# Kernel tuning notes

Measured on AMD Instinct MI355X. Metric: run time of the kernel, lower is better.

## Reference

```python
import jax, jax.numpy as jnp
import numpy as np
from jax import lax

B, T_ENC, IN, H, V, EMB = 128, 512, 2, 256, 29, 8


def _gru_cell(x_t, h, Wih, Whh, bih, bhh):
    # PyTorch GRU cell, gate order (r, z, n)
    gi = x_t @ Wih.T + bih            # [B, 3H]
    gh = h @ Whh.T + bhh              # [B, 3H]
    ir, iz, inn = jnp.split(gi, 3, axis=-1)
    hr, hz, hn = jnp.split(gh, 3, axis=-1)
    r = jax.nn.sigmoid(ir + hr)
    z = jax.nn.sigmoid(iz + hz)
    n = jnp.tanh(inn + r * hn)
    return (1.0 - z) * n + z * h


def _gru_scan(xs, Wih, Whh, bih, bhh, reverse):
    # xs: [B, T, D] -> outputs [B, T, H], final hidden [B, H]
    h0 = jnp.zeros((xs.shape[0], Whh.shape[-1]), xs.dtype)
    def step(h, x_t):
        h = _gru_cell(x_t, h, Wih, Whh, bih, bhh)
        return h, h
    hT, ys = lax.scan(step, h0, jnp.swapaxes(xs, 0, 1), reverse=reverse)
    return jnp.swapaxes(ys, 0, 1), hT


def _forward(x, target_seq, eWih0, eWhh0, ebih0, ebhh0, eWih1, eWhh1, ebih1, ebhh1,
             e2d_W, e2d_b, dWih0, dWih1, dWhh, dbih, dbhh, q_W, q_b, out_W, out_b, emb):
    # ---- bidirectional 2-layer GRU encoder ----
    yf0, hf0 = _gru_scan(x, eWih0[0], eWhh0[0], ebih0[0], ebhh0[0], False)
    yb0, hb0 = _gru_scan(x, eWih0[1], eWhh0[1], ebih0[1], ebhh0[1], True)
    y0 = jnp.concatenate([yf0, yb0], axis=-1)          # [B, T, 2H]
    yf1, hf1 = _gru_scan(y0, eWih1[0], eWhh1[0], ebih1[0], ebhh1[0], False)
    yb1, hb1 = _gru_scan(y0, eWih1[1], eWhh1[1], ebih1[1], ebhh1[1], True)
    y1 = jnp.concatenate([yf1, yb1], axis=-1)          # [B, T, 2H]
    enc_out = y1 @ e2d_W.T + e2d_b                     # [B, T, H]
    # hidden.reshape(L, 2, B, H).sum(dim=1): fwd + bwd per layer
    h0c = hf0 + hb0
    h1c = hf1 + hb1

    max_steps = target_seq.shape[1] - 1
    init_tok = target_seq[:, 0]

    def dec_step(carry, _):
        h0, h1, tok = carry
        e = emb[tok]                                   # [B, EMB]
        h0 = _gru_cell(e, h0, dWih0, dWhh[0], dbih[0], dbhh[0])
        h1 = _gru_cell(h0, h1, dWih1, dWhh[1], dbih[1], dbhh[1])
        q = h1 @ q_W.T + q_b                           # [B, H]
        scores = jnp.einsum('bte,be->bt', enc_out, q)  # [B, T]
        w = jax.nn.softmax(scores, axis=1)
        ctx = jnp.einsum('bt,bte->be', w, enc_out)     # [B, H]
        logits = (h1 + ctx) @ out_W.T + out_b          # [B, V] (dropout is identity in eval)
        tok = jnp.argmax(logits, axis=-1)
        return (h0, h1, tok), logits

    (h0c, h1c, _), logits = lax.scan(dec_step, (h0c, h1c, init_tok), None, length=max_steps)
    logits = jnp.swapaxes(logits, 0, 1)                # [B, max_steps, V]
    hidden = jnp.stack([h0c, h1c], axis=0)             # [L, B, H]
    return logits, hidden


def setup_inputs() -> dict:
    key = jax.random.key(0)
    ks = jax.random.split(key, 24)
    def p(k, *shape):
        return jax.random.normal(k, shape, jnp.float32) * 0.05
    return {
        'x': jax.random.normal(ks[0], (B, T_ENC, IN), jnp.float32),
        'target_seq': jax.random.randint(ks[1], (B, 64), 0, V),
        'eWih0': p(ks[2], 2, 3 * H, IN),
        'eWhh0': p(ks[3], 2, 3 * H, H),
        'ebih0': p(ks[4], 2, 3 * H),
        'ebhh0': p(ks[5], 2, 3 * H),
        'eWih1': p(ks[6], 2, 3 * H, 2 * H),
        'eWhh1': p(ks[7], 2, 3 * H, H),
        'ebih1': p(ks[8], 2, 3 * H),
        'ebhh1': p(ks[9], 2, 3 * H),
        'e2d_W': p(ks[10], H, 2 * H),
        'e2d_b': p(ks[11], H),
        'dWih0': p(ks[12], 3 * H, EMB),
        'dWih1': p(ks[13], 3 * H, H),
        'dWhh': p(ks[14], 2, 3 * H, H),
        'dbih': p(ks[15], 2, 3 * H),
        'dbhh': p(ks[16], 2, 3 * H),
        'q_W': p(ks[17], H, H),
        'q_b': p(ks[18], H),
        'out_W': p(ks[19], V, H),
        'out_b': p(ks[20], V),
        'emb': p(ks[21], V, EMB),
    }


def reference(x, target_seq, eWih0, eWhh0, ebih0, ebhh0, eWih1, eWhh1, ebih1, ebhh1,
              e2d_W, e2d_b, dWih0, dWih1, dWhh, dbih, dbhh, q_W, q_b, out_W, out_b, emb):
    return _forward(x, target_seq, eWih0, eWhh0, ebih0, ebhh0, eWih1, eWhh1, ebih1, ebhh1,
                    e2d_W, e2d_b, dWih0, dWih1, dWhh, dbih, dbhh, q_W, q_b, out_W, out_b, emb)
```

## Files before the change

kernel.cpp:

```cpp
#include <hip/hip_runtime.h>
#include <hip/hip_bf16.h>
#include <hip/hip_fp16.h>
#include <stdint.h>

#define BB 128
#define TT 512
#define HH 256
#define VV 29
#define NSTEP 63
#define BT (BB*TT)
#define CHUNK 64

typedef _Float16 f16;
typedef _Float16 f16x2 __attribute__((ext_vector_type(2)));
typedef _Float16 f16x8 __attribute__((ext_vector_type(8)));
typedef float f32x4 __attribute__((ext_vector_type(4)));

static __device__ __forceinline__ float fdot2u(uint32_t a, uint32_t b, float c) {
  return __builtin_amdgcn_fdot2(__builtin_bit_cast(f16x2, a),
                                __builtin_bit_cast(f16x2, b), c, false);
}
static __device__ __forceinline__ float sigm_(float x) {
  return 1.0f / (1.0f + __expf(-x));
}

__global__ void k_cvt(const float* __restrict__ s, f16* __restrict__ d, int n) {
  int i = blockIdx.x * 256 + threadIdx.x;
  if (i < n) d[i] = (f16)s[i];
}

template<int LAYER>
__global__ __launch_bounds__(512, 2)
void k_scan(const float* __restrict__ x,
            const f16* __restrict__ gi,
            const uint32_t* __restrict__ whh,
            const float* __restrict__ wih0,
            const float* __restrict__ bih,
            const float* __restrict__ bhh,
            f16* __restrict__ y,
            float* __restrict__ hstate,
            int t0, int nsteps)
{
  const int wg = blockIdx.x, b = wg >> 1, dir = wg & 1;
  const int tid = threadIdx.x, pair = tid >> 1, half = tid & 1;
  __shared__ uint32_t hv[128];
  __shared__ float ysh[256];

  uint32_t w0[64], w1[64], w2[64];
  {
    const uint32_t* wp = whh + (size_t)dir * 768 * 128;
    const uint32_t* r0 = wp + (size_t)pair * 128 + half * 64;
    const uint32_t* r1 = wp + (size_t)(pair + 256) * 128 + half * 64;
    const uint32_t* r2 = wp + (size_t)(pair + 512) * 128 + half * 64;
#pragma unroll
    for (int i = 0; i < 64; i++) { w0[i] = r0[i]; w1[i] = r1[i]; w2[i] = r2[i]; }
  }
  const float bh0 = bhh[dir * 768 + pair];
  const float bh1 = bhh[dir * 768 + pair + 256];
  const float bh2 = bhh[dir * 768 + pair + 512];
  float bi0 = 0, bi1 = 0, bi2 = 0;
  float wi00 = 0, wi01 = 0, wi10 = 0, wi11 = 0, wi20 = 0, wi21 = 0;
  if (LAYER == 0) {
    bi0 = bih[dir * 768 + pair];
    bi1 = bih[dir * 768 + pair + 256];
    bi2 = bih[dir * 768 + pair + 512];
    wi00 = wih0[(dir * 768 + pair) * 2 + 0];
    wi01 = wih0[(dir * 768 + pair) * 2 + 1];
    wi10 = wih0[(dir * 768 + pair + 256) * 2 + 0];
    wi11 = wih0[(dir * 768 + pair + 256) * 2 + 1];
    wi20 = wih0[(dir * 768 + pair + 512) * 2 + 0];
    wi21 = wih0[(dir * 768 + pair + 512) * 2 + 1];
  }
  float* hs = hstate + ((size_t)dir * BB + b) * 256;
  float hreg = hs[pair];
  if (tid < 128) {
    f16x2 p2; p2[0] = (f16)hs[2 * tid]; p2[1] = (f16)hs[2 * tid + 1];
    hv[tid] = __builtin_bit_cast(uint32_t, p2);
  }
  __syncthreads();

  for (int s = 0; s < nsteps; ++s) {
    const int t = dir ? (TT - 1 - t0 - s) : (t0 + s);
    float a0 = 0.f, a1 = 0.f, a2 = 0.f;
#pragma unroll
    for (int i = 0; i < 64; i++) {
      uint32_t hh = hv[half * 64 + i];
      a0 = fdot2u(w0[i], hh, a0);
      a1 = fdot2u(w1[i], hh, a1);
      a2 = fdot2u(w2[i], hh, a2);
    }
    a0 += __shfl_xor(a0, 1);
    a1 += __shfl_xor(a1, 1);
    a2 += __shfl_xor(a2, 1);

    float gr, gz, gn;
    if (LAYER == 0) {
      float x0 = x[((size_t)b * TT + t) * 2 + 0];
      float x1 = x[((size_t)b * TT + t) * 2 + 1];
      gr = wi00 * x0 + wi01 * x1 + bi0;
      gz = wi10 * x0 + wi11 * x1 + bi1;
      gn = wi20 * x0 + wi21 * x1 + bi2;
    } else {
      const f16* g = gi + ((size_t)b * nsteps + s) * 1536 + dir * 768 + pair;
      gr = (float)g[0]; gz = (float)g[256]; gn = (float)g[512];
    }
    float r = sigm_(gr + a0 + bh0);
    float z = sigm_(gz + a1 + bh1);
    float n = tanhf(gn + r * (a2 + bh2));
    float hn = (1.0f - z) * n + z * hreg;
    hreg = hn;
    __syncthreads();
    if (half == 0) { ((f16*)hv)[pair] = (f16)hn; ysh[pair] = hn; }
    __syncthreads();
    if (tid < 256) y[((size_t)b * TT + t) * 512 + dir * 256 + tid] = (f16)ysh[tid];
  }
  if (half == 0) hs[pair] = hreg;
}

__global__ __launch_bounds__(256)
void k_gemm(const f16* __restrict__ A, const f16* __restrict__ Bt,
            f16* __restrict__ C, const float* __restrict__ bias,
            int K, int shift, long bstride, int inner, int ldc, int coloff)
{
  const int m0 = blockIdx.x * 64, n0 = blockIdx.y * 64;
  const int tid = threadIdx.x, lane = tid & 63, wv = tid >> 6;
  __shared__ __align__(16) f16 As[64 * 40];
  __shared__ __align__(16) f16 Bs[64 * 40];
  f32x4 acc[4] = {{0,0,0,0},{0,0,0,0},{0,0,0,0},{0,0,0,0}};
  const int lrow = tid >> 2, lseg = tid & 3;
  const int ml = lane & 15, quad = lane >> 4;
  const int r = m0 + lrow;
  const f16* arow = A + (long)(r >> shift) * bstride
                      + (long)(r & ((1 << shift) - 1)) * inner;
  const f16* brow = Bt + (size_t)(n0 + lrow) * K;
  for (int k0 = 0; k0 < K; k0 += 32) {
    uint4 av = *(const uint4*)(arow + k0 + lseg * 8);
    uint4 bv = *(const uint4*)(brow + k0 + lseg * 8);
    __syncthreads();
    *(uint4*)(As + lrow * 40 + lseg * 8) = av;
    *(uint4*)(Bs + lrow * 40 + lseg * 8) = bv;
    __syncthreads();
    f16x8 af = *(const f16x8*)(As + (wv * 16 + ml) * 40 + quad * 8);
#pragma unroll
    for (int ns = 0; ns < 4; ++ns) {
      f16x8 bf = *(const f16x8*)(Bs + (ns * 16 + ml) * 40 + quad * 8);
      acc[ns] = __builtin_amdgcn_mfma_f32_16x16x32_f16(af, bf, acc[ns], 0, 0, 0);
    }
  }
#pragma unroll
  for (int ns = 0; ns < 4; ++ns) {
#pragma unroll
    for (int rr = 0; rr < 4; ++rr) {
      int row = m0 + wv * 16 + quad * 4 + rr;
      int col = n0 + ns * 16 + ml;
      float v = acc[ns][rr];
      if (bias) v += bias[col];
      C[(size_t)row * ldc + coloff + col] = (f16)v;
    }
  }
}

__global__ void k_dinit(const float* __restrict__ hf0, const float* __restrict__ hf1,
                        const int* __restrict__ tseq,
                        f16* __restrict__ h0, f16* __restrict__ h1, int* __restrict__ tok) {
  int i = blockIdx.x * 256 + threadIdx.x;
  h0[i] = (f16)(hf0[i] + hf0[32768 + i]);
  h1[i] = (f16)(hf1[i] + hf1[32768 + i]);
  if (i < BB) tok[i] = tseq[i * 64];
}

__global__ __launch_bounds__(256)
void k_gates0(const f16* __restrict__ wih0,
              const float* __restrict__ bih0,
              const float* __restrict__ emb,
              const int* __restrict__ tok,
              const f16* __restrict__ G,
              const f16* __restrict__ hprev, f16* __restrict__ hnew) {
  int b = blockIdx.x, p = threadIdx.x;
  __shared__ float e[8];
  if (p < 8) e[p] = emb[tok[b] * 8 + p];
  __syncthreads();
  float gr = bih0[p], gz = bih0[p + 256], gn = bih0[p + 512];
#pragma unroll
  for (int i = 0; i < 8; i++) {
    gr += e[i] * (float)wih0[p * 8 + i];
    gz += e[i] * (float)wih0[(p + 256) * 8 + i];
    gn += e[i] * (float)wih0[(p + 512) * 8 + i];
  }
  const f16* g = G + b * 768;
  float r = sigm_(gr + (float)g[p]);
  float z = sigm_(gz + (float)g[p + 256]);
  float n = tanhf(gn + r * (float)g[p + 512]);
  float hp = (float)hprev[b * 256 + p];
  hnew[b * 256 + p] = (f16)((1.f - z) * n + z * hp);
}

__global__ __launch_bounds__(256)
void k_gates1(const f16* __restrict__ Ga, const f16* __restrict__ Gb,
              const f16* __restrict__ hprev, f16* __restrict__ hnew) {
  int b = blockIdx.x, p = threadIdx.x;
  const f16* ga = Ga + b * 768;
  const f16* gb = Gb + b * 768;
  float r = sigm_((float)ga[p] + (float)gb[p]);
  float z = sigm_((float)ga[p + 256] + (float)gb[p + 256]);
  float n = tanhf((float)ga[p + 512] + r * (float)gb[p + 512]);
  float hp = (float)hprev[b * 256 + p];
  hnew[b * 256 + p] = (f16)((1.f - z) * n + z * hp);
}

__global__ __launch_bounds__(256)
void k_attn(const f16* __restrict__ enc,
            const f16* __restrict__ q,
            const f16* __restrict__ h1,
            const f16* __restrict__ outw,
            const float* __restrict__ outb,
            float* __restrict__ dlogits, int* __restrict__ tok, int step) {
  int b = blockIdx.x, tid = threadIdx.x;
  __shared__ uint32_t qs[128];
  __shared__ float sc[512];
  __shared__ float red[4];
  __shared__ float hc[256];
  __shared__ float lg[32];
  if (tid < 128) qs[tid] = ((const uint32_t*)q)[b * 128 + tid];
  __syncthreads();
#pragma unroll
  for (int pass = 0; pass < 2; ++pass) {
    int t = tid + pass * 256;
    const uint4* ep = (const uint4*)(enc + ((size_t)b * TT + t) * 256);
    float s = 0.f;
#pragma unroll
    for (int j = 0; j < 32; j++) {
      uint4 v = ep[j];
      s = fdot2u(v.x, qs[j * 4 + 0], s);
      s = fdot2u(v.y, qs[j * 4 + 1], s);
      s = fdot2u(v.z, qs[j * 4 + 2], s);
      s = fdot2u(v.w, qs[j * 4 + 3], s);
    }
    sc[t] = s;
  }
  __syncthreads();
  float mloc = fmaxf(sc[tid], sc[tid + 256]);
#pragma unroll
  for (int off = 32; off; off >>= 1) mloc = fmaxf(mloc, __shfl_xor(mloc, off));
  if ((tid & 63) == 0) red[tid >> 6] = mloc;
  __syncthreads();
  float m = fmaxf(fmaxf(red[0], red[1]), fmaxf(red[2], red[3]));
  float e0 = __expf(sc[tid] - m), e1 = __expf(sc[tid + 256] - m);
  __syncthreads();
  sc[tid] = e0; sc[tid + 256] = e1;
  float lloc = e0 + e1;
#pragma unroll
  for (int off = 32; off; off >>= 1) lloc += __shfl_xor(lloc, off);
  if ((tid & 63) == 0) red[tid >> 6] = lloc;
  __syncthreads();
  float l = red[0] + red[1] + red[2] + red[3];
  float ctx = 0.f;
#pragma unroll 4
  for (int t = 0; t < TT; t++) ctx += sc[t] * (float)enc[((size_t)b * TT + t) * 256 + tid];
  ctx /= l;
  hc[tid] = ctx + (float)h1[b * 256 + tid];
  __syncthreads();
  if (tid < VV) {
    float acc = outb[tid];
    const f16* ow = outw + tid * 256;
    for (int k = 0; k < 256; k++) acc += hc[k] * (float)ow[k];
    lg[tid] = acc;
    dlogits[((size_t)b * NSTEP + step) * VV + tid] = acc;
  }
  __syncthreads();
  if (tid == 0) {
    int best = 0; float bv = lg[0];
    for (int v = 1; v < VV; ++v) if (lg[v] > bv) { bv = lg[v]; best = v; }
    tok[b] = best;
  }
}

__global__ void k_fin(const f16* __restrict__ h0, const f16* __restrict__ h1,
                      float* __restrict__ out) {
  int i = blockIdx.x * 256 + threadIdx.x;
  out[233856 + i] = (float)(i < 32768 ? h0[i] : h1[i - 32768]);
}

extern "C" void kernel_launch(void* const* d_in, const int* in_sizes, int n_in,
                              void* d_out, int out_size, void* d_ws, size_t ws_size,
                              hipStream_t stream) {
  (void)in_sizes; (void)n_in; (void)out_size; (void)ws_size;
  const float* x     = (const float*)d_in[0];
  const int*   tseq  = (const int*)d_in[1];
  const float* eWih0 = (const float*)d_in[2];
  const float* eWhh0 = (const float*)d_in[3];
  const float* ebih0 = (const float*)d_in[4];
  const float* ebhh0 = (const float*)d_in[5];
  const float* eWih1 = (const float*)d_in[6];
  const float* eWhh1 = (const float*)d_in[7];
  const float* ebih1 = (const float*)d_in[8];
  const float* ebhh1 = (const float*)d_in[9];
  const float* e2dW  = (const float*)d_in[10];
  const float* e2db  = (const float*)d_in[11];
  const float* dWih0 = (const float*)d_in[12];
  const float* dWih1 = (const float*)d_in[13];
  const float* dWhh  = (const float*)d_in[14];
  const float* dbih  = (const float*)d_in[15];
  const float* dbhh  = (const float*)d_in[16];
  const float* qW    = (const float*)d_in[17];
  const float* qb    = (const float*)d_in[18];
  const float* outW  = (const float*)d_in[19];
  const float* outb  = (const float*)d_in[20];
  const float* emb   = (const float*)d_in[21];

  uint8_t* ws = (uint8_t*)d_ws;
  size_t o = 0;
  auto take = [&](size_t bytes) -> void* {
    void* p = ws + o;
    o += (bytes + 255) & ~(size_t)255;
    return p;
  };
  f16* whh0_16  = (f16*)take((size_t)2 * 768 * 256 * 2);
  f16* whh1_16  = (f16*)take((size_t)2 * 768 * 256 * 2);
  f16* wih1_16  = (f16*)take((size_t)2 * 768 * 512 * 2);
  f16* e2d_16   = (f16*)take((size_t)256 * 512 * 2);
  f16* qw_16    = (f16*)take((size_t)256 * 256 * 2);
  f16* outw_16  = (f16*)take((size_t)29 * 256 * 2);
  f16* dwih0_16 = (f16*)take((size_t)768 * 8 * 2);
  f16* dwih1_16 = (f16*)take((size_t)768 * 256 * 2);
  f16* dwhh_16  = (f16*)take((size_t)2 * 768 * 256 * 2);
  f16* y0   = (f16*)take((size_t)BT * 512 * 2);
  f16* y1   = (f16*)take((size_t)BT * 512 * 2);
  f16* gi   = (f16*)take((size_t)BB * CHUNK * 1536 * 2);
  float* hs0 = (float*)take((size_t)2 * BB * 256 * 4);
  float* hs1 = (float*)take((size_t)2 * BB * 256 * 4);
  f16* qbuf = (f16*)take((size_t)BB * 256 * 2);
  f16* h0buf[2] = { (f16*)take((size_t)BB * 256 * 2), (f16*)take((size_t)BB * 256 * 2) };
  f16* h1buf[2] = { (f16*)take((size_t)BB * 256 * 2), (f16*)take((size_t)BB * 256 * 2) };
  f16* G0  = (f16*)take((size_t)BB * 768 * 2);
  f16* G1a = (f16*)take((size_t)BB * 768 * 2);
  f16* G1b = (f16*)take((size_t)BB * 768 * 2);
  int* tok = (int*)take((size_t)BB * 4);
  f16* enc = y0;

  hipMemsetAsync(hs0, 0, (size_t)2 * BB * 256 * 4, stream);
  hipMemsetAsync(hs1, 0, (size_t)2 * BB * 256 * 4, stream);

  auto cvt = [&](const float* s, f16* d, int n) {
    k_cvt<<<(n + 255) / 256, 256, 0, stream>>>(s, d, n);
  };
  cvt(eWhh0, whh0_16, 2 * 768 * 256);
  cvt(eWhh1, whh1_16, 2 * 768 * 256);
  cvt(eWih1, wih1_16, 2 * 768 * 512);
  cvt(e2dW,  e2d_16,  256 * 512);
  cvt(qW,    qw_16,   256 * 256);
  cvt(outW,  outw_16, 29 * 256);
  cvt(dWih0, dwih0_16, 768 * 8);
  cvt(dWih1, dwih1_16, 768 * 256);
  cvt(dWhh,  dwhh_16, 2 * 768 * 256);

  k_scan<0><<<256, 512, 0, stream>>>(x, nullptr, (const uint32_t*)whh0_16,
                                     eWih0, ebih0, ebhh0, y0, hs0, 0, TT);

  const long BSTR = (long)TT * 512;
  for (int c = 0; c < TT / CHUNK; ++c) {
    const int t0 = c * CHUNK;
    k_gemm<<<dim3(BB * CHUNK / 64, 12), 256, 0, stream>>>(
        y0 + (size_t)t0 * 512, wih1_16, gi, ebih1,
        512, 6, BSTR, 512, 1536, 0);
    k_gemm<<<dim3(BB * CHUNK / 64, 12), 256, 0, stream>>>(
        y0 + (size_t)(TT - 1 - t0) * 512, wih1_16 + (size_t)768 * 512, gi, ebih1 + 768,
        512, 6, BSTR, -512, 1536, 768);
    k_scan<1><<<256, 512, 0, stream>>>(nullptr, gi, (const uint32_t*)whh1_16,
                                       nullptr, nullptr, ebhh1, y1, hs1, t0, CHUNK);
  }

  k_gemm<<<dim3(BT / 64, 4), 256, 0, stream>>>(y1, e2d_16, enc, e2db,
                                               512, 30, 0, 512, 256, 0);
  k_dinit<<<128, 256, 0, stream>>>(hs0, hs1, tseq, h0buf[0], h1buf[0], tok);

  int cur = 0;
  for (int s = 0; s < NSTEP; ++s) {
    int nxt = cur ^ 1;
    k_gemm<<<dim3(2, 12), 256, 0, stream>>>(h0buf[cur], dwhh_16, G0, dbhh,
                                            256, 30, 0, 256, 768, 0);
    k_gates0<<<128, 256, 0, stream>>>(dwih0_16, dbih, emb, tok, G0,
                                      h0buf[cur], h0buf[nxt]);
    k_gemm<<<dim3(2, 12), 256, 0, stream>>>(h0buf[nxt], dwih1_16, G1a, dbih + 768,
                                            256, 30, 0, 256, 768, 0);
    k_gemm<<<dim3(2, 12), 256, 0, stream>>>(h1buf[cur], dwhh_16 + (size_t)768 * 256,
                                            G1b, dbhh + 768, 256, 30, 0, 256, 768, 0);
    k_gates1<<<128, 256, 0, stream>>>(G1a, G1b, h1buf[cur], h1buf[nxt]);
    k_gemm<<<dim3(2, 4), 256, 0, stream>>>(h1buf[nxt], qw_16, qbuf, qb,
                                           256, 30, 0, 256, 256, 0);
    k_attn<<<128, 256, 0, stream>>>(enc, qbuf, h1buf[nxt], outw_16, outb,
                                    (float*)d_out, tok, s);
    cur = nxt;
  }
  k_fin<<<256, 256, 0, stream>>>(h0buf[cur], h1buf[cur], (float*)d_out);
}
```

Baseline: 6.358 ms.

## Fuse decoder loop into one persistent kernel and vectorize encoder scan

The whole 63-step autoregressive decoder (GRU cells, query projection, attention, output logits, argmax) moves into a single kernel with one block per batch row. This replaces roughly 440 small launches and the global round-trips of gates and hidden states between them. In exchange, every block re-reads the full decoder weight matrices from global/L2 each step with matrix-vector dot products instead of MFMA GEMMs. The encoder scan also switches to uint4 weight registers and vector LDS reads, and writes y directly, dropping one shared staging buffer.

```diff
diff --git a/kernel.cpp b/kernel.cpp
--- a/kernel.cpp
+++ b/kernel.cpp
@@ -43,17 +43,16 @@
 {
   const int wg = blockIdx.x, b = wg >> 1, dir = wg & 1;
   const int tid = threadIdx.x, pair = tid >> 1, half = tid & 1;
-  __shared__ uint32_t hv[128];
-  __shared__ float ysh[256];
-
-  uint32_t w0[64], w1[64], w2[64];
+  __shared__ __align__(16) uint4 hv4[32];
+
+  uint4 w0[16], w1[16], w2[16];
   {
     const uint32_t* wp = whh + (size_t)dir * 768 * 128;
-    const uint32_t* r0 = wp + (size_t)pair * 128 + half * 64;
-    const uint32_t* r1 = wp + (size_t)(pair + 256) * 128 + half * 64;
-    const uint32_t* r2 = wp + (size_t)(pair + 512) * 128 + half * 64;
-#pragma unroll
-    for (int i = 0; i < 64; i++) { w0[i] = r0[i]; w1[i] = r1[i]; w2[i] = r2[i]; }
+    const uint4* r0 = (const uint4*)(wp + (size_t)pair * 128 + half * 64);
+    const uint4* r1 = (const uint4*)(wp + (size_t)(pair + 256) * 128 + half * 64);
+    const uint4* r2 = (const uint4*)(wp + (size_t)(pair + 512) * 128 + half * 64);
+#pragma unroll
+    for (int i = 0; i < 16; i++) { w0[i] = r0[i]; w1[i] = r1[i]; w2[i] = r2[i]; }
   }
   const float bh0 = bhh[dir * 768 + pair];
   const float bh1 = bhh[dir * 768 + pair + 256];
@@ -75,24 +74,13 @@
   float hreg = hs[pair];
   if (tid < 128) {
     f16x2 p2; p2[0] = (f16)hs[2 * tid]; p2[1] = (f16)hs[2 * tid + 1];
-    hv[tid] = __builtin_bit_cast(uint32_t, p2);
+    ((uint32_t*)hv4)[tid] = __builtin_bit_cast(uint32_t, p2);
   }
   __syncthreads();
 
+  const uint4* hw = hv4 + half * 16;
   for (int s = 0; s < nsteps; ++s) {
     const int t = dir ? (TT - 1 - t0 - s) : (t0 + s);
-    float a0 = 0.f, a1 = 0.f, a2 = 0.f;
-#pragma unroll
-    for (int i = 0; i < 64; i++) {
-      uint32_t hh = hv[half * 64 + i];
-      a0 = fdot2u(w0[i], hh, a0);
-      a1 = fdot2u(w1[i], hh, a1);
-      a2 = fdot2u(w2[i], hh, a2);
-    }
-    a0 += __shfl_xor(a0, 1);
-    a1 += __shfl_xor(a1, 1);
-    a2 += __shfl_xor(a2, 1);
-
     float gr, gz, gn;
     if (LAYER == 0) {
       float x0 = x[((size_t)b * TT + t) * 2 + 0];
@@ -104,15 +92,30 @@
       const f16* g = gi + ((size_t)b * nsteps + s) * 1536 + dir * 768 + pair;
       gr = (float)g[0]; gz = (float)g[256]; gn = (float)g[512];
     }
+    float a0 = 0.f, a1 = 0.f, a2 = 0.f;
+#pragma unroll
+    for (int j = 0; j < 16; ++j) {
+      uint4 hh = hw[j];
+      a0 = fdot2u(w0[j].x, hh.x, a0); a0 = fdot2u(w0[j].y, hh.y, a0);
+      a0 = fdot2u(w0[j].z, hh.z, a0); a0 = fdot2u(w0[j].w, hh.w, a0);
+      a1 = fdot2u(w1[j].x, hh.x, a1); a1 = fdot2u(w1[j].y, hh.y, a1);
+      a1 = fdot2u(w1[j].z, hh.z, a1); a1 = fdot2u(w1[j].w, hh.w, a1);
+      a2 = fdot2u(w2[j].x, hh.x, a2); a2 = fdot2u(w2[j].y, hh.y, a2);
+      a2 = fdot2u(w2[j].z, hh.z, a2); a2 = fdot2u(w2[j].w, hh.w, a2);
+    }
+    a0 += __shfl_xor(a0, 1);
+    a1 += __shfl_xor(a1, 1);
+    a2 += __shfl_xor(a2, 1);
+
     float r = sigm_(gr + a0 + bh0);
     float z = sigm_(gz + a1 + bh1);
     float n = tanhf(gn + r * (a2 + bh2));
     float hn = (1.0f - z) * n + z * hreg;
     hreg = hn;
-    __syncthreads();
-    if (half == 0) { ((f16*)hv)[pair] = (f16)hn; ysh[pair] = hn; }
-    __syncthreads();
-    if (tid < 256) y[((size_t)b * TT + t) * 512 + dir * 256 + tid] = (f16)ysh[tid];
+    if (half == 0) y[((size_t)b * TT + t) * 512 + dir * 256 + pair] = (f16)hn;
+    __syncthreads();
+    if (half == 0) ((f16*)hv4)[pair] = (f16)hn;
+    __syncthreads();
   }
   if (half == 0) hs[pair] = hreg;
 }
@@ -160,125 +163,203 @@
   }
 }
 
-__global__ void k_dinit(const float* __restrict__ hf0, const float* __restrict__ hf1,
-                        const int* __restrict__ tseq,
-                        f16* __restrict__ h0, f16* __restrict__ h1, int* __restrict__ tok) {
-  int i = blockIdx.x * 256 + threadIdx.x;
-  h0[i] = (f16)(hf0[i] + hf0[32768 + i]);
-  h1[i] = (f16)(hf1[i] + hf1[32768 + i]);
-  if (i < BB) tok[i] = tseq[i * 64];
+static __device__ __forceinline__ void mv3(const f16* __restrict__ W, int row0,
+                                           const uint4* __restrict__ hsh,
+                                           float& g0, float& g1, float& g2) {
+  const uint4* w0 = (const uint4*)(W + (size_t)row0 * 256);
+  const uint4* w1 = (const uint4*)(W + (size_t)(row0 + 256) * 256);
+  const uint4* w2 = (const uint4*)(W + (size_t)(row0 + 512) * 256);
+#pragma unroll 2
+  for (int kc = 0; kc < 8; ++kc) {
+    uint4 hq[4], aq[4], bq[4], cq[4];
+#pragma unroll
+    for (int j = 0; j < 4; ++j) {
+      aq[j] = w0[4 * kc + j]; bq[j] = w1[4 * kc + j]; cq[j] = w2[4 * kc + j];
+      hq[j] = hsh[4 * kc + j];
+    }
+#pragma unroll
+    for (int j = 0; j < 4; ++j) {
+      g0 = fdot2u(aq[j].x, hq[j].x, g0); g0 = fdot2u(aq[j].y, hq[j].y, g0);
+      g0 = fdot2u(aq[j].z, hq[j].z, g0); g0 = fdot2u(aq[j].w, hq[j].w, g0);
+      g1 = fdot2u(bq[j].x, hq[j].x, g1); g1 = fdot2u(bq[j].y, hq[j].y, g1);
+      g1 = fdot2u(bq[j].z, hq[j].z, g1); g1 = fdot2u(bq[j].w, hq[j].w, g1);
+      g2 = fdot2u(cq[j].x, hq[j].x, g2); g2 = fdot2u(cq[j].y, hq[j].y, g2);
+      g2 = fdot2u(cq[j].z, hq[j].z, g2); g2 = fdot2u(cq[j].w, hq[j].w, g2);
+    }
+  }
+}
+static __device__ __forceinline__ float mv1(const f16* __restrict__ W, long row,
+                                            const uint4* __restrict__ hsh, float g) {
+  const uint4* w = (const uint4*)(W + (size_t)row * 256);
+#pragma unroll 2
+  for (int kc = 0; kc < 8; ++kc) {
+    uint4 aq[4], hq[4];
+#pragma unroll
+    for (int j = 0; j < 4; ++j) { aq[j] = w[4 * kc + j]; hq[j] = hsh[4 * kc + j]; }
+#pragma unroll
+    for (int j = 0; j < 4; ++j) {
+      g = fdot2u(aq[j].x, hq[j].x, g); g = fdot2u(aq[j].y, hq[j].y, g);
+      g = fdot2u(aq[j].z, hq[j].z, g); g = fdot2u(aq[j].w, hq[j].w, g);
+    }
+  }
+  return g;
+}
+static __device__ __forceinline__ float edot(uint4 w, const float* e) {
+  f16x2 a = __builtin_bit_cast(f16x2, w.x);
+  f16x2 b = __builtin_bit_cast(f16x2, w.y);
+  f16x2 c = __builtin_bit_cast(f16x2, w.z);
+  f16x2 d = __builtin_bit_cast(f16x2, w.w);
+  return (float)a[0]*e[0] + (float)a[1]*e[1] + (float)b[0]*e[2] + (float)b[1]*e[3]
+       + (float)c[0]*e[4] + (float)c[1]*e[5] + (float)d[0]*e[6] + (float)d[1]*e[7];
 }
 
 __global__ __launch_bounds__(256)
-void k_gates0(const f16* __restrict__ wih0,
-              const float* __restrict__ bih0,
-              const float* __restrict__ emb,
-              const int* __restrict__ tok,
-              const f16* __restrict__ G,
-              const f16* __restrict__ hprev, f16* __restrict__ hnew) {
-  int b = blockIdx.x, p = threadIdx.x;
-  __shared__ float e[8];
-  if (p < 8) e[p] = emb[tok[b] * 8 + p];
-  __syncthreads();
-  float gr = bih0[p], gz = bih0[p + 256], gn = bih0[p + 512];
-#pragma unroll
-  for (int i = 0; i < 8; i++) {
-    gr += e[i] * (float)wih0[p * 8 + i];
-    gz += e[i] * (float)wih0[(p + 256) * 8 + i];
-    gn += e[i] * (float)wih0[(p + 512) * 8 + i];
-  }
-  const f16* g = G + b * 768;
-  float r = sigm_(gr + (float)g[p]);
-  float z = sigm_(gz + (float)g[p + 256]);
-  float n = tanhf(gn + r * (float)g[p + 512]);
-  float hp = (float)hprev[b * 256 + p];
-  hnew[b * 256 + p] = (f16)((1.f - z) * n + z * hp);
-}
-
-__global__ __launch_bounds__(256)
-void k_gates1(const f16* __restrict__ Ga, const f16* __restrict__ Gb,
-              const f16* __restrict__ hprev, f16* __restrict__ hnew) {
-  int b = blockIdx.x, p = threadIdx.x;
-  const f16* ga = Ga + b * 768;
-  const f16* gb = Gb + b * 768;
-  float r = sigm_((float)ga[p] + (float)gb[p]);
-  float z = sigm_((float)ga[p + 256] + (float)gb[p + 256]);
-  float n = tanhf((float)ga[p + 512] + r * (float)gb[p + 512]);
-  float hp = (float)hprev[b * 256 + p];
-  hnew[b * 256 + p] = (f16)((1.f - z) * n + z * hp);
-}
-
-__global__ __launch_bounds__(256)
-void k_attn(const f16* __restrict__ enc,
-            const f16* __restrict__ q,
-            const f16* __restrict__ h1,
-            const f16* __restrict__ outw,
-            const float* __restrict__ outb,
-            float* __restrict__ dlogits, int* __restrict__ tok, int step) {
-  int b = blockIdx.x, tid = threadIdx.x;
-  __shared__ uint32_t qs[128];
+void k_decoder(const f16* __restrict__ dwhh,
+               const f16* __restrict__ dwih1,
+               const f16* __restrict__ dwih0,
+               const f16* __restrict__ qw,
+               const f16* __restrict__ outw,
+               const f16* __restrict__ enc,
+               const float* __restrict__ dbih,
+               const float* __restrict__ dbhh,
+               const float* __restrict__ qb, const float* __restrict__ outb,
+               const float* __restrict__ emb,
+               const float* __restrict__ hs0, const float* __restrict__ hs1,
+               const int* __restrict__ tseq,
+               float* __restrict__ out)
+{
+  const int b = blockIdx.x, tid = threadIdx.x;
+  __shared__ __align__(16) f16 h0sh[256], h1sh[256], qsh[256];
   __shared__ float sc[512];
   __shared__ float red[4];
-  __shared__ float hc[256];
+  __shared__ __align__(16) float hc[256];
+  __shared__ __align__(16) float cpart[2][256];
   __shared__ float lg[32];
-  if (tid < 128) qs[tid] = ((const uint32_t*)q)[b * 128 + tid];
+  __shared__ float e8[8];
+  __shared__ int toksh;
+
+  h0sh[tid] = (f16)(hs0[b * 256 + tid] + hs0[32768 + b * 256 + tid]);
+  h1sh[tid] = (f16)(hs1[b * 256 + tid] + hs1[32768 + b * 256 + tid]);
+  if (tid == 0) toksh = tseq[b * 64];
   __syncthreads();
-#pragma unroll
-  for (int pass = 0; pass < 2; ++pass) {
-    int t = tid + pass * 256;
-    const uint4* ep = (const uint4*)(enc + ((size_t)b * TT + t) * 256);
-    float s = 0.f;
-#pragma unroll
-    for (int j = 0; j < 32; j++) {
-      uint4 v = ep[j];
-      s = fdot2u(v.x, qs[j * 4 + 0], s);
-      s = fdot2u(v.y, qs[j * 4 + 1], s);
-      s = fdot2u(v.z, qs[j * 4 + 2], s);
-      s = fdot2u(v.w, qs[j * 4 + 3], s);
-    }
-    sc[t] = s;
-  }
-  __syncthreads();
-  float mloc = fmaxf(sc[tid], sc[tid + 256]);
-#pragma unroll
-  for (int off = 32; off; off >>= 1) mloc = fmaxf(mloc, __shfl_xor(mloc, off));
-  if ((tid & 63) == 0) red[tid >> 6] = mloc;
-  __syncthreads();
-  float m = fmaxf(fmaxf(red[0], red[1]), fmaxf(red[2], red[3]));
-  float e0 = __expf(sc[tid] - m), e1 = __expf(sc[tid + 256] - m);
-  __syncthreads();
-  sc[tid] = e0; sc[tid + 256] = e1;
-  float lloc = e0 + e1;
-#pragma unroll
-  for (int off = 32; off; off >>= 1) lloc += __shfl_xor(lloc, off);
-  if ((tid & 63) == 0) red[tid >> 6] = lloc;
-  __syncthreads();
-  float l = red[0] + red[1] + red[2] + red[3];
-  float ctx = 0.f;
-#pragma unroll 4
-  for (int t = 0; t < TT; t++) ctx += sc[t] * (float)enc[((size_t)b * TT + t) * 256 + tid];
-  ctx /= l;
-  hc[tid] = ctx + (float)h1[b * 256 + tid];
-  __syncthreads();
-  if (tid < VV) {
-    float acc = outb[tid];
-    const f16* ow = outw + tid * 256;
-    for (int k = 0; k < 256; k++) acc += hc[k] * (float)ow[k];
-    lg[tid] = acc;
-    dlogits[((size_t)b * NSTEP + step) * VV + tid] = acc;
-  }
-  __syncthreads();
-  if (tid == 0) {
-    int best = 0; float bv = lg[0];
-    for (int v = 1; v < VV; ++v) if (lg[v] > bv) { bv = lg[v]; best = v; }
-    tok[b] = best;
-  }
-}
-
-__global__ void k_fin(const f16* __restrict__ h0, const f16* __restrict__ h1,
-                      float* __restrict__ out) {
-  int i = blockIdx.x * 256 + threadIdx.x;
-  out[233856 + i] = (float)(i < 32768 ? h0[i] : h1[i - 32768]);
+
+  for (int s = 0; s < NSTEP; ++s) {
+    if (tid < 8) e8[tid] = emb[toksh * 8 + tid];
+    uint4 wq0 = *(const uint4*)(dwih0 + (size_t)tid * 8);
+    uint4 wq1 = *(const uint4*)(dwih0 + (size_t)(tid + 256) * 8);
+    uint4 wq2 = *(const uint4*)(dwih0 + (size_t)(tid + 512) * 8);
+    float g0 = dbhh[tid], g1 = dbhh[tid + 256], g2 = dbhh[tid + 512];
+    mv3(dwhh, tid, (const uint4*)h0sh, g0, g1, g2);
+    __syncthreads();
+    {
+      float i0 = dbih[tid]       + edot(wq0, e8);
+      float i1 = dbih[tid + 256] + edot(wq1, e8);
+      float i2 = dbih[tid + 512] + edot(wq2, e8);
+      float r = sigm_(i0 + g0);
+      float z = sigm_(i1 + g1);
+      float n = tanhf(i2 + r * g2);
+      float hp = (float)h0sh[tid];
+      h0sh[tid] = (f16)((1.f - z) * n + z * hp);
+    }
+    __syncthreads();
+
+    float a0 = dbih[768 + tid], a1 = dbih[768 + tid + 256], a2 = dbih[768 + tid + 512];
+    mv3(dwih1, tid, (const uint4*)h0sh, a0, a1, a2);
+    float b0 = dbhh[768 + tid], b1 = dbhh[768 + tid + 256], b2 = dbhh[768 + tid + 512];
+    mv3(dwhh + (size_t)768 * 256, tid, (const uint4*)h1sh, b0, b1, b2);
+    float h1new;
+    {
+      float r = sigm_(a0 + b0);
+      float z = sigm_(a1 + b1);
+      float n = tanhf(a2 + r * b2);
+      float hp = (float)h1sh[tid];
+      h1new = (1.f - z) * n + z * hp;
+    }
+    __syncthreads();
+    h1sh[tid] = (f16)h1new;
+    __syncthreads();
+
+    qsh[tid] = (f16)mv1(qw, tid, (const uint4*)h1sh, qb[tid]);
+    __syncthreads();
+
+#pragma unroll
+    for (int pass = 0; pass < 2; ++pass) {
+      int t = tid + pass * 256;
+      sc[t] = mv1(enc, (size_t)b * 512 + t, (const uint4*)qsh, 0.f);
+    }
+    __syncthreads();
+
+    float mloc = fmaxf(sc[tid], sc[tid + 256]);
+#pragma unroll
+    for (int off = 32; off; off >>= 1) mloc = fmaxf(mloc, __shfl_xor(mloc, off));
+    if ((tid & 63) == 0) red[tid >> 6] = mloc;
+    __syncthreads();
+    float m = fmaxf(fmaxf(red[0], red[1]), fmaxf(red[2], red[3]));
+    float ex0 = __expf(sc[tid] - m), ex1 = __expf(sc[tid + 256] - m);
+    __syncthreads();
+    sc[tid] = ex0; sc[tid + 256] = ex1;
+    float lloc = ex0 + ex1;
+#pragma unroll
+    for (int off = 32; off; off >>= 1) lloc += __shfl_xor(lloc, off);
+    if ((tid & 63) == 0) red[tid >> 6] = lloc;
+    __syncthreads();
+    float l = red[0] + red[1] + red[2] + red[3];
+
+    {
+      const int c2 = tid & 127, th = tid >> 7;
+      const uint32_t* eb = (const uint32_t*)enc + (((size_t)b * 512 + th * 256) * 128) + c2;
+      const float* wsc = sc + th * 256;
+      float c0 = 0.f, c1 = 0.f;
+#pragma unroll 8
+      for (int i = 0; i < 256; ++i) {
+        uint32_t v = eb[(size_t)i * 128];
+        float wgt = wsc[i];
+        f16x2 h2 = __builtin_bit_cast(f16x2, v);
+        c0 += wgt * (float)h2[0];
+        c1 += wgt * (float)h2[1];
+      }
+      ((float2*)cpart[th])[c2] = float2{c0, c1};
+    }
+    __syncthreads();
+    hc[tid] = (cpart[0][tid] + cpart[1][tid]) / l + (float)h1sh[tid];
+    __syncthreads();
+
+    if (tid < VV * 8) {
+      const int v = tid >> 3, kseg = tid & 7;
+      float acc = 0.f;
+      const uint4* ow = (const uint4*)(outw + (size_t)v * 256 + kseg * 32);
+      const float4* hv = (const float4*)(hc + kseg * 32);
+#pragma unroll
+      for (int j = 0; j < 4; ++j) {
+        uint4 wq = ow[j];
+        float4 ha = hv[2 * j], hb = hv[2 * j + 1];
+        f16x2 p0 = __builtin_bit_cast(f16x2, wq.x);
+        f16x2 p1 = __builtin_bit_cast(f16x2, wq.y);
+        f16x2 p2 = __builtin_bit_cast(f16x2, wq.z);
+        f16x2 p3 = __builtin_bit_cast(f16x2, wq.w);
+        acc += (float)p0[0]*ha.x + (float)p0[1]*ha.y + (float)p1[0]*ha.z + (float)p1[1]*ha.w;
+        acc += (float)p2[0]*hb.x + (float)p2[1]*hb.y + (float)p3[0]*hb.z + (float)p3[1]*hb.w;
+      }
+      acc += __shfl_xor(acc, 1);
+      acc += __shfl_xor(acc, 2);
+      acc += __shfl_xor(acc, 4);
+      if (kseg == 0) {
+        float lv = acc + outb[v];
+        lg[v] = lv;
+        out[((size_t)b * NSTEP + s) * VV + v] = lv;
+      }
+    }
+    __syncthreads();
+    if (tid == 0) {
+      int best = 0; float bv = lg[0];
+      for (int v = 1; v < VV; ++v) if (lg[v] > bv) { bv = lg[v]; best = v; }
+      toksh = best;
+    }
+    __syncthreads();
+  }
+
+  out[233856 + b * 256 + tid] = (float)h0sh[tid];
+  out[233856 + 32768 + b * 256 + tid] = (float)h1sh[tid];
 }
 
 extern "C" void kernel_launch(void* const* d_in, const int* in_sizes, int n_in,
@@ -329,13 +410,6 @@
   f16* gi   = (f16*)take((size_t)BB * CHUNK * 1536 * 2);
   float* hs0 = (float*)take((size_t)2 * BB * 256 * 4);
   float* hs1 = (float*)take((size_t)2 * BB * 256 * 4);
-  f16* qbuf = (f16*)take((size_t)BB * 256 * 2);
-  f16* h0buf[2] = { (f16*)take((size_t)BB * 256 * 2), (f16*)take((size_t)BB * 256 * 2) };
-  f16* h1buf[2] = { (f16*)take((size_t)BB * 256 * 2), (f16*)take((size_t)BB * 256 * 2) };
-  f16* G0  = (f16*)take((size_t)BB * 768 * 2);
-  f16* G1a = (f16*)take((size_t)BB * 768 * 2);
-  f16* G1b = (f16*)take((size_t)BB * 768 * 2);
-  int* tok = (int*)take((size_t)BB * 4);
   f16* enc = y0;
 
   hipMemsetAsync(hs0, 0, (size_t)2 * BB * 256 * 4, stream);
@@ -372,25 +446,8 @@
 
   k_gemm<<<dim3(BT / 64, 4), 256, 0, stream>>>(y1, e2d_16, enc, e2db,
                                                512, 30, 0, 512, 256, 0);
-  k_dinit<<<128, 256, 0, stream>>>(hs0, hs1, tseq, h0buf[0], h1buf[0], tok);
-
-  int cur = 0;
-  for (int s = 0; s < NSTEP; ++s) {
-    int nxt = cur ^ 1;
-    k_gemm<<<dim3(2, 12), 256, 0, stream>>>(h0buf[cur], dwhh_16, G0, dbhh,
-                                            256, 30, 0, 256, 768, 0);
-    k_gates0<<<128, 256, 0, stream>>>(dwih0_16, dbih, emb, tok, G0,
-                                      h0buf[cur], h0buf[nxt]);
-    k_gemm<<<dim3(2, 12), 256, 0, stream>>>(h0buf[nxt], dwih1_16, G1a, dbih + 768,
-                                            256, 30, 0, 256, 768, 0);
-    k_gemm<<<dim3(2, 12), 256, 0, stream>>>(h1buf[cur], dwhh_16 + (size_t)768 * 256,
-                                            G1b, dbhh + 768, 256, 30, 0, 256, 768, 0);
-    k_gates1<<<128, 256, 0, stream>>>(G1a, G1b, h1buf[cur], h1buf[nxt]);
-    k_gemm<<<dim3(2, 4), 256, 0, stream>>>(h1buf[nxt], qw_16, qbuf, qb,
-                                           256, 30, 0, 256, 256, 0);
-    k_attn<<<128, 256, 0, stream>>>(enc, qbuf, h1buf[nxt], outw_16, outb,
-                                    (float*)d_out, tok, s);
-    cur = nxt;
-  }
-  k_fin<<<256, 256, 0, stream>>>(h0buf[cur], h1buf[cur], (float*)d_out);
-}
+
+  k_decoder<<<128, 256, 0, stream>>>(dwhh_16, dwih1_16, dwih0_16, qw_16, outw_16,
+                                     enc, dbih, dbhh, qb, outb, emb,
+                                     hs0, hs1, tseq, (float*)d_out);
+}
```

Measured after the change: 5.571 ms. -12.4%, faster.
